# Performance work log

Measured on AMD Instinct MI355X. Metric: run time of the kernel, lower is better.

The kernel has to match this reference:

```python
import jax, jax.numpy as jnp
import numpy as np

D = 2048  # filter_dim
B = 4096  # tokens per TTT step


def setup_inputs() -> dict:
    key = jax.random.key(0)
    ks = jax.random.split(key, 8)
    s = 1.0 / np.sqrt(D)  # kaiming-ish scale so activations stay O(1)
    return {
        "src": jax.random.normal(ks[0], (B, D), jnp.float32),
        "theta_k": jax.random.normal(ks[1], (D, D), jnp.float32) * s,
        "theta_q": jax.random.normal(ks[2], (D, D), jnp.float32) * s,
        "theta_v": jax.random.normal(ks[3], (D, D), jnp.float32) * s,
        "W": jax.random.normal(ks[4], (D, D), jnp.float32) * s,
        "b": jnp.zeros((D,), jnp.float32),
        "lr_w": jax.random.uniform(ks[5], (D, D), jnp.float32) * 0.1,
        "lr_b": jax.random.uniform(ks[6], (D,), jnp.float32) * 0.1,
    }


def reference(src, theta_k, theta_q, theta_v, W, b, lr_w, lr_b):
    # Projections: src is [B, D], thetas are [D, D]
    train_view = src @ theta_k           # [B, D]
    label_view = src @ theta_v           # [B, D]
    test_view = src @ theta_q            # [B, D]

    target = label_view - train_view     # reconstruction target
    pred = train_view @ W.T + b          # nn.Linear(train_view)
    err = pred - target                  # [B, D]

    # Analytic grads of MSELoss (mean over B*D elements) wrt W ([D,D]) and b ([D])
    n = err.size  # B * D (static)
    coef = 2.0 / n
    gW = coef * (err.T @ train_view)     # [D, D], matches w.weight layout
    gb = coef * jnp.sum(err, axis=0)     # [D]

    # Per-element learning-rate SGD step (the in-place parameter rewrite)
    W_new = W - lr_w * gW
    b_new = b - lr_b * gb

    # Query with updated weights + residual
    z = test_view @ W_new.T + b_new + test_view
    return z
```

## Files before the change

### kernel.cpp

```cpp
#include <hip/hip_runtime.h>
#include <hip/hip_bf16.h>
#include <hip/hip_fp8.h>
#include <stdint.h>

#define D_DIM 2048
#define B_TOK 4096
#define COEF (2.0f / 8388608.0f)

typedef __bf16 bf16x8 __attribute__((ext_vector_type(8)));
typedef float  f32x4  __attribute__((ext_vector_type(4)));
typedef int    i32x8  __attribute__((ext_vector_type(8)));

__device__ __forceinline__ unsigned short f2bf(float f) {
  return __builtin_bit_cast(unsigned short, (__bf16)f);
}
__device__ __forceinline__ float bf2f(unsigned short u) {
  return (float)__builtin_bit_cast(__bf16, u);
}
__device__ __forceinline__ unsigned char f2f8(float f) {
  __hip_fp8_e4m3 v(f);
  return v.__x;
}

__device__ __forceinline__ void async16(const void* g, void* l) {
  __builtin_amdgcn_global_load_lds(
      (__attribute__((address_space(1))) void*)(g),
      (__attribute__((address_space(3))) void*)(l),
      16, 0, 0);
}

__device__ __forceinline__ void gemm_core_256(const unsigned short* __restrict__ Ablk,
                                              const unsigned short* __restrict__ Bblk,
                                              const int lda, const int ldb, const int KC,
                                              unsigned short* As, unsigned short* Bs,
                                              f32x4 acc[4][4]) {
  const int tid  = threadIdx.x;
  const int lane = tid & 63;
  const int wv   = tid >> 6;
  const int wm   = wv >> 1;
  const int wn   = wv & 1;
  const int t    = lane & 15;
  const int quad = lane >> 4;
  const int lrow = lane >> 3;
  const int kq   = lane & 7;
  const int kqs  = kq ^ lrow;

  const int nk = KC >> 6;

  auto stageA2 = [&](int buf, int kt, int l0) {
    const int k0 = kt << 6;
    unsigned short* Ad = As + buf * 16384;
#pragma unroll
    for (int l = l0; l < l0 + 2; ++l) {
      const int seg = wv * 4 + l;
      const int r   = seg * 8 + lrow;
      async16(Ablk + (size_t)r * lda + k0 + kqs * 8, Ad + seg * 512);
    }
  };
  auto stageB1 = [&](int buf, int kt, int l) {
    const int k0 = kt << 6;
    unsigned short* Bd = Bs + buf * 8192;
    const int seg = wv * 2 + l;
    const int r   = seg * 8 + lrow;
    async16(Bblk + (size_t)r * ldb + k0 + kqs * 8, Bd + seg * 512);
  };

  stageA2(0, 0, 0); stageA2(0, 0, 2); stageB1(0, 0, 0); stageB1(0, 0, 1);
  if (nk > 1) { stageA2(1, 1, 0); stageA2(1, 1, 2); stageB1(1, 1, 0); stageB1(1, 1, 1); }
  if (nk > 1) asm volatile("s_waitcnt vmcnt(6)" ::: "memory");
  else        asm volatile("s_waitcnt vmcnt(0)" ::: "memory");
  __builtin_amdgcn_s_barrier();

  int cur = 0;
  for (int kt = 0; kt < nk; ++kt) {
    const unsigned short* Ac = As + cur * 16384;
    const unsigned short* Bc = Bs + cur * 8192;
    const int nb = (cur >= 1) ? cur - 1 : 2;
    const bool pf = (kt + 2 < nk);

    bf16x8 af[4], bfr[4];
#pragma unroll
    for (int i = 0; i < 4; ++i) {
      const int rm = wm * 64 + i * 16 + t;
      af[i]  = *(const bf16x8*)(Ac + rm * 64 + ((quad) ^ (rm & 7)) * 8);
      const int rn = wn * 64 + i * 16 + t;
      bfr[i] = *(const bf16x8*)(Bc + rn * 64 + ((quad) ^ (rn & 7)) * 8);
    }
    __builtin_amdgcn_sched_barrier(0);
    if (pf) { stageA2(nb, kt + 2, 0); stageB1(nb, kt + 2, 0); }
    __builtin_amdgcn_sched_barrier(0);
    __builtin_amdgcn_s_barrier();
    asm volatile("s_waitcnt lgkmcnt(0)" ::: "memory");
    __builtin_amdgcn_sched_barrier(0);
    __builtin_amdgcn_s_setprio(1);
#pragma unroll
    for (int i = 0; i < 4; ++i)
#pragma unroll
      for (int j = 0; j < 4; ++j)
        acc[i][j] = __builtin_amdgcn_mfma_f32_16x16x32_bf16(af[i], bfr[j], acc[i][j], 0, 0, 0);
    __builtin_amdgcn_s_setprio(0);
    __builtin_amdgcn_sched_barrier(0);
    __builtin_amdgcn_s_barrier();

#pragma unroll
    for (int i = 0; i < 4; ++i) {
      const int rm = wm * 64 + i * 16 + t;
      af[i]  = *(const bf16x8*)(Ac + rm * 64 + ((4 + quad) ^ (rm & 7)) * 8);
      const int rn = wn * 64 + i * 16 + t;
      bfr[i] = *(const bf16x8*)(Bc + rn * 64 + ((4 + quad) ^ (rn & 7)) * 8);
    }
    __builtin_amdgcn_sched_barrier(0);
    if (pf) { stageA2(nb, kt + 2, 2); stageB1(nb, kt + 2, 1); }
    __builtin_amdgcn_sched_barrier(0);
    if (pf)               asm volatile("s_waitcnt vmcnt(6)" ::: "memory");
    else if (kt + 1 < nk) asm volatile("s_waitcnt vmcnt(0)" ::: "memory");
    __builtin_amdgcn_s_barrier();
    asm volatile("s_waitcnt lgkmcnt(0)" ::: "memory");
    __builtin_amdgcn_sched_barrier(0);
    __builtin_amdgcn_s_setprio(1);
#pragma unroll
    for (int i = 0; i < 4; ++i)
#pragma unroll
      for (int j = 0; j < 4; ++j)
        acc[i][j] = __builtin_amdgcn_mfma_f32_16x16x32_bf16(af[i], bfr[j], acc[i][j], 0, 0, 0);
    __builtin_amdgcn_s_setprio(0);
    __builtin_amdgcn_sched_barrier(0);
    __builtin_amdgcn_s_barrier();

    cur = (cur == 2) ? 0 : cur + 1;
  }
}

#define GEMM_PROLOGUE256(AP, BP, LDAv, LDBv, KCv)                              \
  __shared__ __align__(16) unsigned short As[3 * 16384];                       \
  __shared__ __align__(16) unsigned short Bs[3 * 8192];                        \
  const int lin = blockIdx.y * 16 + blockIdx.x;                                \
  const int swz = (lin & 7) * 32 + (lin >> 3);                                 \
  const int bx = swz & 15, by = swz >> 4;                                      \
  const unsigned short* Ablk = (AP) + (size_t)by * 256 * (LDAv);               \
  const unsigned short* Bblk = (BP) + (size_t)bx * 128 * (LDBv);               \
  f32x4 acc[4][4];                                                             \
  _Pragma("unroll") for (int i = 0; i < 4; ++i)                                \
  _Pragma("unroll") for (int j = 0; j < 4; ++j)                                \
      acc[i][j] = (f32x4){0.f, 0.f, 0.f, 0.f};                                 \
  gemm_core_256(Ablk, Bblk, (LDAv), (LDBv), (KCv), As, Bs, acc);               \
  const int lane = threadIdx.x & 63;                                           \
  const int wv = threadIdx.x >> 6;                                             \
  const int wm = wv >> 1, wn = wv & 1;                                         \
  const int t = lane & 15, quad = lane >> 4;                                   \
  const int gm_base = by * 256 + wm * 64;                                      \
  const int gn_base = bx * 128 + wn * 64;

__device__ __forceinline__ void gemm_core_f8_256(const unsigned char* __restrict__ Ablk,
                                                 const unsigned char* __restrict__ Bblk,
                                                 const int lda, const int ldb, const int KC,
                                                 unsigned char* As, unsigned char* Bs,
                                                 f32x4 acc[4][4]) {
  const int tid  = threadIdx.x;
  const int lane = tid & 63;
  const int wv   = tid >> 6;
  const int wm   = wv >> 1;
  const int wn   = wv & 1;
  const int t    = lane & 15;
  const int quad = lane >> 4;
  const int lrow = lane >> 3;
  const int kq   = lane & 7;
  const int kqs  = kq ^ lrow;

  const int nk = KC >> 7;

  auto stageA2 = [&](int buf, int kt, int l0) {
    const int k0 = kt << 7;
    unsigned char* Ad = As + buf * 32768;
#pragma unroll
    for (int l = l0; l < l0 + 2; ++l) {
      const int seg = wv * 4 + l;
      const int r   = seg * 8 + lrow;
      async16(Ablk + (size_t)r * lda + k0 + kqs * 16, Ad + seg * 1024);
    }
  };
  auto stageB1 = [&](int buf, int kt, int l) {
    const int k0 = kt << 7;
    unsigned char* Bd = Bs + buf * 16384;
    const int seg = wv * 2 + l;
    const int r   = seg * 8 + lrow;
    async16(Bblk + (size_t)r * ldb + k0 + kqs * 16, Bd + seg * 1024);
  };

  auto readF = [&](const unsigned char* base, int x) -> i32x8 {
    const uint4 lo = *(const uint4*)(base + (((quad << 1)    ) ^ x) * 16);
    const uint4 hi = *(const uint4*)(base + (((quad << 1) | 1) ^ x) * 16);
    return (i32x8){(int)lo.x, (int)lo.y, (int)lo.z, (int)lo.w,
                   (int)hi.x, (int)hi.y, (int)hi.z, (int)hi.w};
  };

  stageA2(0, 0, 0); stageA2(0, 0, 2); stageB1(0, 0, 0); stageB1(0, 0, 1);
  if (nk > 1) { stageA2(1, 1, 0); stageA2(1, 1, 2); stageB1(1, 1, 0); stageB1(1, 1, 1); }
  if (nk > 1) asm volatile("s_waitcnt vmcnt(6)" ::: "memory");
  else        asm volatile("s_waitcnt vmcnt(0)" ::: "memory");
  __builtin_amdgcn_s_barrier();

  int cur = 0;
  for (int kt = 0; kt < nk; ++kt) {
    const unsigned char* Ac = As + cur * 32768;
    const unsigned char* Bc = Bs + cur * 16384;
    const int nb = (cur >= 1) ? cur - 1 : 2;
    const bool pf = (kt + 2 < nk);

    i32x8 af[4], bq0, bq1;
#pragma unroll
    for (int i = 0; i < 4; ++i) {
      const int rm = wm * 64 + i * 16 + t;
      af[i] = readF(Ac + rm * 128, rm & 7);
    }
    {
      const int rn0 = wn * 64 + 0 * 16 + t;
      bq0 = readF(Bc + rn0 * 128, rn0 & 7);
      const int rn1 = wn * 64 + 1 * 16 + t;
      bq1 = readF(Bc + rn1 * 128, rn1 & 7);
    }
    __builtin_amdgcn_sched_barrier(0);
    if (pf) { stageA2(nb, kt + 2, 0); stageB1(nb, kt + 2, 0); }
    __builtin_amdgcn_sched_barrier(0);
    __builtin_amdgcn_s_barrier();
    asm volatile("s_waitcnt lgkmcnt(0)" ::: "memory");
    __builtin_amdgcn_sched_barrier(0);
    __builtin_amdgcn_s_setprio(1);
#pragma unroll
    for (int i = 0; i < 4; ++i) {
      acc[i][0] = __builtin_amdgcn_mfma_scale_f32_16x16x128_f8f6f4(
          af[i], bq0, acc[i][0], 0, 0, 0, 127, 0, 127);
      acc[i][1] = __builtin_amdgcn_mfma_scale_f32_16x16x128_f8f6f4(
          af[i], bq1, acc[i][1], 0, 0, 0, 127, 0, 127);
    }
    __builtin_amdgcn_s_setprio(0);
    __builtin_amdgcn_sched_barrier(0);
    __builtin_amdgcn_s_barrier();

    {
      const int rn2 = wn * 64 + 2 * 16 + t;
      bq0 = readF(Bc + rn2 * 128, rn2 & 7);
      const int rn3 = wn * 64 + 3 * 16 + t;
      bq1 = readF(Bc + rn3 * 128, rn3 & 7);
    }
    __builtin_amdgcn_sched_barrier(0);
    if (pf) { stageA2(nb, kt + 2, 2); stageB1(nb, kt + 2, 1); }
    __builtin_amdgcn_sched_barrier(0);
    if (pf)               asm volatile("s_waitcnt vmcnt(6)" ::: "memory");
    else if (kt + 1 < nk) asm volatile("s_waitcnt vmcnt(0)" ::: "memory");
    __builtin_amdgcn_s_barrier();
    asm volatile("s_waitcnt lgkmcnt(0)" ::: "memory");
    __builtin_amdgcn_sched_barrier(0);
    __builtin_amdgcn_s_setprio(1);
#pragma unroll
    for (int i = 0; i < 4; ++i) {
      acc[i][2] = __builtin_amdgcn_mfma_scale_f32_16x16x128_f8f6f4(
          af[i], bq0, acc[i][2], 0, 0, 0, 127, 0, 127);
      acc[i][3] = __builtin_amdgcn_mfma_scale_f32_16x16x128_f8f6f4(
          af[i], bq1, acc[i][3], 0, 0, 0, 127, 0, 127);
    }
    __builtin_amdgcn_s_setprio(0);
    __builtin_amdgcn_sched_barrier(0);
    __builtin_amdgcn_s_barrier();

    cur = (cur == 2) ? 0 : cur + 1;
  }
}

#define GEMM8_PROLOGUE256(AP, BP, LDAv, LDBv, KCv)                             \
  __shared__ __align__(16) unsigned char As8[3 * 32768];                       \
  __shared__ __align__(16) unsigned char Bs8[3 * 16384];                       \
  const int nwg = gridDim.x * gridDim.y;                                       \
  const int lin = blockIdx.y * 16 + blockIdx.x;                                \
  const int swz = (lin & 7) * (nwg >> 3) + (lin >> 3);                         \
  const int bx = swz & 15, by = swz >> 4;                                      \
  const unsigned char* Ablk = (AP) + (size_t)by * 256 * (LDAv);                \
  const unsigned char* Bblk = (BP) + (size_t)bx * 128 * (LDBv);                \
  f32x4 acc[4][4];                                                             \
  _Pragma("unroll") for (int i = 0; i < 4; ++i)                                \
  _Pragma("unroll") for (int j = 0; j < 4; ++j)                                \
      acc[i][j] = (f32x4){0.f, 0.f, 0.f, 0.f};                                 \
  gemm_core_f8_256(Ablk, Bblk, (LDAv), (LDBv), (KCv), As8, Bs8, acc);          \
  const int lane = threadIdx.x & 63;                                           \
  const int wv = threadIdx.x >> 6;                                             \
  const int wm = wv >> 1, wn = wv & 1;                                         \
  const int t = lane & 15, quad = lane >> 4;                                   \
  const int gm_base = by * 256 + wm * 64;                                      \
  const int gn_base = bx * 128 + wn * 64;

__global__ __launch_bounds__(512, 2) void gemm_train_f8(
    const unsigned char* __restrict__ srcA,
    const unsigned char* __restrict__ thkT8,
    unsigned char* __restrict__ src_cat_f8,
    unsigned char* __restrict__ trainT8) {
  GEMM8_PROLOGUE256(srcA, thkT8, 4096, 2048, 2048)
  unsigned char* scr = As8 + wv * 2304;
#pragma unroll
  for (int p = 0; p < 2; ++p) {
#pragma unroll
    for (int jl = 0; jl < 2; ++jl) {
      const int j = p * 2 + jl;
      const int gn = gn_base + j * 16 + t;
#pragma unroll
      for (int i = 0; i < 4; ++i) {
        const int gm0 = gm_base + i * 16 + quad * 4;
        uchar4 pk = make_uchar4(f2f8(acc[i][j][0]), f2f8(acc[i][j][1]),
                                f2f8(acc[i][j][2]), f2f8(acc[i][j][3]));
        src_cat_f8[(size_t)(gm0 + 0) * 4096 + gn] = pk.x;
        src_cat_f8[(size_t)(gm0 + 1) * 4096 + gn] = pk.y;
        src_cat_f8[(size_t)(gm0 + 2) * 4096 + gn] = pk.z;
        src_cat_f8[(size_t)(gm0 + 3) * 4096 + gn] = pk.w;
        *(uchar4*)(scr + (jl * 16 + t) * 72 + i * 16 + quad * 4) = pk;
      }
    }
    __syncthreads();
    const int row = lane >> 3, chunk = lane & 7;
#pragma unroll
    for (int q = 0; q < 4; ++q) {
      const int rr = q * 8 + row;
      const uint2 v = *(const uint2*)(scr + rr * 72 + chunk * 8);
      *(uint2*)(trainT8 + (size_t)(gn_base + p * 32 + rr) * B_TOK + gm_base + chunk * 8) = v;
    }
    __syncthreads();
  }
}

__global__ __launch_bounds__(512, 2) void gemm_test(
    const unsigned short* __restrict__ src_bf,
    const unsigned short* __restrict__ thqT,
    unsigned short* __restrict__ testv) {
  GEMM_PROLOGUE256(src_bf, thqT, 2048, 2048, 2048)
#pragma unroll
  for (int i = 0; i < 4; ++i) {
#pragma unroll
    for (int j = 0; j < 4; ++j) {
      const int gm0 = gm_base + i * 16 + quad * 4;
      const int gn  = gn_base + j * 16 + t;
#pragma unroll
      for (int r = 0; r < 4; ++r)
        testv[(size_t)(gm0 + r) * D_DIM + gn] = f2bf(acc[i][j][r]);
    }
  }
}

__global__ __launch_bounds__(512, 2) void gemm_err_f8(
    const unsigned char* __restrict__ src_cat_f8,
    const unsigned char* __restrict__ Wcat_f8,
    const float* __restrict__ bvec,
    unsigned char* __restrict__ errT8,
    float* __restrict__ gb) {
  GEMM8_PROLOGUE256(src_cat_f8, Wcat_f8, 4096, 4096, 4096)
  unsigned char* scr = As8 + wv * 2304;
#pragma unroll
  for (int p = 0; p < 2; ++p) {
#pragma unroll
    for (int jl = 0; jl < 2; ++jl) {
      const int j = p * 2 + jl;
      const int gn = gn_base + j * 16 + t;
      const float bias = bvec[gn];
      float cs = 0.f;
#pragma unroll
      for (int i = 0; i < 4; ++i) {
        const float e0 = acc[i][j][0] + bias, e1 = acc[i][j][1] + bias;
        const float e2 = acc[i][j][2] + bias, e3 = acc[i][j][3] + bias;
        *(uchar4*)(scr + (jl * 16 + t) * 72 + i * 16 + quad * 4) =
            make_uchar4(f2f8(e0), f2f8(e1), f2f8(e2), f2f8(e3));
        cs += e0 + e1 + e2 + e3;
      }
      cs += __shfl_xor(cs, 16);
      cs += __shfl_xor(cs, 32);
      if (quad == 0) atomicAdd(&gb[gn], cs);
    }
    __syncthreads();
    const int row = lane >> 3, chunk = lane & 7;
#pragma unroll
    for (int q = 0; q < 4; ++q) {
      const int rr = q * 8 + row;
      const uint2 v = *(const uint2*)(scr + rr * 72 + chunk * 8);
      *(uint2*)(errT8 + (size_t)(gn_base + p * 32 + rr) * B_TOK + gm_base + chunk * 8) = v;
    }
    __syncthreads();
  }
}

__global__ __launch_bounds__(512, 2) void gemm_gw_f8(
    const unsigned char* __restrict__ errT8,
    const unsigned char* __restrict__ trainT8,
    float* __restrict__ P0, float* __restrict__ P1) {
  const int z = blockIdx.z;
  const unsigned char* Abase = errT8 + z * 2048;
  const unsigned char* Bbase = trainT8 + z * 2048;
  GEMM8_PROLOGUE256(Abase, Bbase, B_TOK, B_TOK, 2048)
  float* P = (z == 0) ? P0 : P1;
#pragma unroll
  for (int i = 0; i < 4; ++i) {
#pragma unroll
    for (int j = 0; j < 4; ++j) {
      const int gm0 = gm_base + i * 16 + quad * 4;
      const int gn  = gn_base + j * 16 + t;
#pragma unroll
      for (int r = 0; r < 4; ++r)
        P[(size_t)(gm0 + r) * D_DIM + gn] = acc[i][j][r];
    }
  }
}

__global__ __launch_bounds__(256) void wnew_reduce(
    const float* __restrict__ P0, const float* __restrict__ P1,
    const float* __restrict__ W, const float* __restrict__ lr_w,
    unsigned short* __restrict__ Wnew) {
  const int i = blockIdx.x * 256 + threadIdx.x;
  const float4 p0 = ((const float4*)P0)[i];
  const float4 p1 = ((const float4*)P1)[i];
  const float4 w  = ((const float4*)W)[i];
  const float4 l  = ((const float4*)lr_w)[i];
  ((ushort4*)Wnew)[i] = make_ushort4(
      f2bf(w.x - l.x * (COEF * (p0.x + p1.x))),
      f2bf(w.y - l.y * (COEF * (p0.y + p1.y))),
      f2bf(w.z - l.z * (COEF * (p0.z + p1.z))),
      f2bf(w.w - l.w * (COEF * (p0.w + p1.w))));
}

__global__ __launch_bounds__(512, 2) void gemm_out(
    const unsigned short* __restrict__ testv,
    const unsigned short* __restrict__ Wnew,
    const float* __restrict__ bvec,
    const float* __restrict__ lr_b,
    const float* __restrict__ gb,
    float* __restrict__ out) {
  GEMM_PROLOGUE256(testv, Wnew, 2048, 2048, 2048)
#pragma unroll
  for (int j = 0; j < 4; ++j) {
    const int gn = gn_base + j * 16 + t;
    const float bias = bvec[gn] - lr_b[gn] * (COEF * gb[gn]);
#pragma unroll
    for (int i = 0; i < 4; ++i) {
      const int gm0 = gm_base + i * 16 + quad * 4;
#pragma unroll
      for (int r = 0; r < 4; ++r) {
        const size_t idx = (size_t)(gm0 + r) * D_DIM + gn;
        out[idx] = acc[i][j][r] + bias + bf2f(testv[idx]);
      }
    }
  }
}

__global__ __launch_bounds__(256) void cvt_all(const float* __restrict__ src,
                                               const float* __restrict__ W,
                                               unsigned short* __restrict__ src_bf,
                                               unsigned char* __restrict__ src_cat_f8,
                                               unsigned char* __restrict__ Wcat_f8,
                                               float* __restrict__ gb) {
  const int i = blockIdx.x * 256 + threadIdx.x;
  if (i < 512) ((float4*)gb)[i] = (float4){0.f, 0.f, 0.f, 0.f};
  if (i < 2097152) {
    const int m = i >> 9, c = i & 511;
    const float4 v = ((const float4*)src)[i];
    ((ushort4*)src_bf)[i] = make_ushort4(f2bf(v.x), f2bf(v.y), f2bf(v.z), f2bf(v.w));
    *(uchar4*)(src_cat_f8 + (size_t)m * 4096 + 2048 + c * 4) =
        make_uchar4(f2f8(v.x), f2f8(v.y), f2f8(v.z), f2f8(v.w));
  } else {
    const int j = i - 2097152;
    const int n = j >> 9, c = j & 511;
    const float4 v = ((const float4*)W)[j];
    *(uchar4*)(Wcat_f8 + (size_t)n * 4096 + c * 4) =
        make_uchar4(f2f8(v.x), f2f8(v.y), f2f8(v.z), f2f8(v.w));
  }
}

__global__ __launch_bounds__(256) void tcvt(
    const float* __restrict__ thk, const float* __restrict__ thq,
    const float* __restrict__ thv,
    unsigned char* __restrict__ thkT8, unsigned short* __restrict__ thqT,
    unsigned char* __restrict__ Wcat_f8) {
  __shared__ float tile[32][33];
  const int z = blockIdx.z;
  const int bx = blockIdx.x * 32, by = blockIdx.y * 32;
  const int tx = threadIdx.x & 31, ty = threadIdx.x >> 5;
#pragma unroll
  for (int l = 0; l < 4; ++l) {
    const int r = ty + l * 8;
    const size_t idx = (size_t)(by + r) * D_DIM + bx + tx;
    tile[r][tx] = (z == 0) ? thk[idx] : (z == 1) ? thq[idx] : (thk[idx] - thv[idx]);
  }
  __syncthreads();
#pragma unroll
  for (int l = 0; l < 4; ++l) {
    const int r = ty + l * 8;
    if (z == 0)
      thkT8[(size_t)(bx + r) * 2048 + by + tx] = f2f8(tile[tx][r]);
    else if (z == 1)
      thqT[(size_t)(bx + r) * 2048 + by + tx] = f2bf(tile[tx][r]);
    else
      Wcat_f8[(size_t)(bx + r) * 4096 + 2048 + by + tx] = f2f8(tile[tx][r]);
  }
}

extern "C" void kernel_launch(void* const* d_in, const int* in_sizes, int n_in,
                              void* d_out, int out_size, void* d_ws, size_t ws_size,
                              hipStream_t stream) {
  const float* src = (const float*)d_in[0];
  const float* thk = (const float*)d_in[1];
  const float* thq = (const float*)d_in[2];
  const float* thv = (const float*)d_in[3];
  const float* W   = (const float*)d_in[4];
  const float* bv  = (const float*)d_in[5];
  const float* lrw = (const float*)d_in[6];
  const float* lrb = (const float*)d_in[7];
  float* out = (float*)d_out;

  char* ws = (char*)d_ws;
  const size_t MB = 1024 * 1024;
  unsigned short* src_bf     = (unsigned short*)(ws + 0);
  unsigned char*  src_cat_f8 = (unsigned char*)(ws + 16 * MB);
  unsigned char*  Wcat_f8    = (unsigned char*)(ws + 32 * MB);
  unsigned char*  thkT8      = (unsigned char*)(ws + 40 * MB);
  unsigned short* thqT       = (unsigned short*)(ws + 44 * MB);
  unsigned char*  trainT8    = (unsigned char*)(ws + 52 * MB);
  unsigned short* testv      = (unsigned short*)(ws + 60 * MB);
  unsigned char*  errT8      = (unsigned char*)(ws + 76 * MB);
  unsigned short* WnewBf     = (unsigned short*)(ws + 84 * MB);
  float*          P0         = (float*)(ws + 92 * MB);
  float*          P1         = (float*)(ws + 108 * MB);
  float*          gb         = (float*)(ws + 124 * MB);

  cvt_all<<<12288, 256, 0, stream>>>(src, W, src_bf, src_cat_f8, Wcat_f8, gb);
  tcvt<<<dim3(64, 64, 3), 256, 0, stream>>>(thk, thq, thv, thkT8, thqT, Wcat_f8);

  gemm_train_f8<<<dim3(16, 16), 512, 0, stream>>>(src_cat_f8 + 2048, thkT8,
                                                  src_cat_f8, trainT8);
  gemm_test<<<dim3(16, 16), 512, 0, stream>>>(src_bf, thqT, testv);
  gemm_err_f8<<<dim3(16, 16), 512, 0, stream>>>(src_cat_f8, Wcat_f8, bv, errT8, gb);
  gemm_gw_f8<<<dim3(16, 8, 2), 512, 0, stream>>>(errT8, trainT8, P0, P1);
  wnew_reduce<<<4096, 256, 0, stream>>>(P0, P1, W, lrw, WnewBf);
  gemm_out<<<dim3(16, 16), 512, 0, stream>>>(testv, WnewBf, bv, lrb, gb, out);
}
```

Measured before the change: 335.7 us.

## Cut barriers per k-step by reading full LDS tile before MFMA phases

In both the bf16 and fp8 GEMM cores, each k-iteration now reads all fragments for both sub-phases from LDS up front, issues all global prefetches at once, and runs the two MFMA groups separated only by partial lgkmcnt waits. This takes the per-iteration workgroup barriers from four down to one. It is meant to remove barrier stalls and let LDS reads overlap the first MFMA group. The cost is higher register pressure from the doubled fragment arrays. Safety with the triple buffer now depends on the single remaining barrier.

```diff
diff --git a/kernel.cpp b/kernel.cpp
--- a/kernel.cpp
+++ b/kernel.cpp
@@ -78,55 +78,49 @@
     const int nb = (cur >= 1) ? cur - 1 : 2;
     const bool pf = (kt + 2 < nk);
 
-    bf16x8 af[4], bfr[4];
+    bf16x8 af0[4], bf0[4], af1[4], bf1[4];
 #pragma unroll
     for (int i = 0; i < 4; ++i) {
       const int rm = wm * 64 + i * 16 + t;
-      af[i]  = *(const bf16x8*)(Ac + rm * 64 + ((quad) ^ (rm & 7)) * 8);
       const int rn = wn * 64 + i * 16 + t;
-      bfr[i] = *(const bf16x8*)(Bc + rn * 64 + ((quad) ^ (rn & 7)) * 8);
-    }
-    __builtin_amdgcn_sched_barrier(0);
-    if (pf) { stageA2(nb, kt + 2, 0); stageB1(nb, kt + 2, 0); }
-    __builtin_amdgcn_sched_barrier(0);
-    __builtin_amdgcn_s_barrier();
-    asm volatile("s_waitcnt lgkmcnt(0)" ::: "memory");
-    __builtin_amdgcn_sched_barrier(0);
-    __builtin_amdgcn_s_setprio(1);
-#pragma unroll
-    for (int i = 0; i < 4; ++i)
-#pragma unroll
-      for (int j = 0; j < 4; ++j)
-        acc[i][j] = __builtin_amdgcn_mfma_f32_16x16x32_bf16(af[i], bfr[j], acc[i][j], 0, 0, 0);
-    __builtin_amdgcn_s_setprio(0);
-    __builtin_amdgcn_sched_barrier(0);
-    __builtin_amdgcn_s_barrier();
-
+      af0[i] = *(const bf16x8*)(Ac + rm * 64 + ((quad) ^ (rm & 7)) * 8);
+      bf0[i] = *(const bf16x8*)(Bc + rn * 64 + ((quad) ^ (rn & 7)) * 8);
+    }
+    __builtin_amdgcn_sched_barrier(0);
 #pragma unroll
     for (int i = 0; i < 4; ++i) {
       const int rm = wm * 64 + i * 16 + t;
-      af[i]  = *(const bf16x8*)(Ac + rm * 64 + ((4 + quad) ^ (rm & 7)) * 8);
       const int rn = wn * 64 + i * 16 + t;
-      bfr[i] = *(const bf16x8*)(Bc + rn * 64 + ((4 + quad) ^ (rn & 7)) * 8);
-    }
-    __builtin_amdgcn_sched_barrier(0);
-    if (pf) { stageA2(nb, kt + 2, 2); stageB1(nb, kt + 2, 1); }
+      af1[i] = *(const bf16x8*)(Ac + rm * 64 + ((4 + quad) ^ (rm & 7)) * 8);
+      bf1[i] = *(const bf16x8*)(Bc + rn * 64 + ((4 + quad) ^ (rn & 7)) * 8);
+    }
+    __builtin_amdgcn_sched_barrier(0);
+    if (pf) { stageA2(nb, kt + 2, 0); stageA2(nb, kt + 2, 2);
+              stageB1(nb, kt + 2, 0); stageB1(nb, kt + 2, 1); }
+    __builtin_amdgcn_sched_barrier(0);
+    asm volatile("s_waitcnt lgkmcnt(8)" ::: "memory");
+    __builtin_amdgcn_sched_barrier(0);
+    __builtin_amdgcn_s_setprio(1);
+#pragma unroll
+    for (int i = 0; i < 4; ++i)
+#pragma unroll
+      for (int j = 0; j < 4; ++j)
+        acc[i][j] = __builtin_amdgcn_mfma_f32_16x16x32_bf16(af0[i], bf0[j], acc[i][j], 0, 0, 0);
+    __builtin_amdgcn_s_setprio(0);
+    __builtin_amdgcn_sched_barrier(0);
+    asm volatile("s_waitcnt lgkmcnt(0)" ::: "memory");
+    __builtin_amdgcn_sched_barrier(0);
+    __builtin_amdgcn_s_setprio(1);
+#pragma unroll
+    for (int i = 0; i < 4; ++i)
+#pragma unroll
+      for (int j = 0; j < 4; ++j)
+        acc[i][j] = __builtin_amdgcn_mfma_f32_16x16x32_bf16(af1[i], bf1[j], acc[i][j], 0, 0, 0);
+    __builtin_amdgcn_s_setprio(0);
     __builtin_amdgcn_sched_barrier(0);
     if (pf)               asm volatile("s_waitcnt vmcnt(6)" ::: "memory");
     else if (kt + 1 < nk) asm volatile("s_waitcnt vmcnt(0)" ::: "memory");
     __builtin_amdgcn_s_barrier();
-    asm volatile("s_waitcnt lgkmcnt(0)" ::: "memory");
-    __builtin_amdgcn_sched_barrier(0);
-    __builtin_amdgcn_s_setprio(1);
-#pragma unroll
-    for (int i = 0; i < 4; ++i)
-#pragma unroll
-      for (int j = 0; j < 4; ++j)
-        acc[i][j] = __builtin_amdgcn_mfma_f32_16x16x32_bf16(af[i], bfr[j], acc[i][j], 0, 0, 0);
-    __builtin_amdgcn_s_setprio(0);
-    __builtin_amdgcn_sched_barrier(0);
-    __builtin_amdgcn_s_barrier();
-
     cur = (cur == 2) ? 0 : cur + 1;
   }
 }
@@ -207,7 +201,7 @@
     const int nb = (cur >= 1) ? cur - 1 : 2;
     const bool pf = (kt + 2 < nk);
 
-    i32x8 af[4], bq0, bq1;
+    i32x8 af[4], bq0, bq1, bq2, bq3;
 #pragma unroll
     for (int i = 0; i < 4; ++i) {
       const int rm = wm * 64 + i * 16 + t;
@@ -220,10 +214,17 @@
       bq1 = readF(Bc + rn1 * 128, rn1 & 7);
     }
     __builtin_amdgcn_sched_barrier(0);
-    if (pf) { stageA2(nb, kt + 2, 0); stageB1(nb, kt + 2, 0); }
-    __builtin_amdgcn_sched_barrier(0);
-    __builtin_amdgcn_s_barrier();
-    asm volatile("s_waitcnt lgkmcnt(0)" ::: "memory");
+    {
+      const int rn2 = wn * 64 + 2 * 16 + t;
+      bq2 = readF(Bc + rn2 * 128, rn2 & 7);
+      const int rn3 = wn * 64 + 3 * 16 + t;
+      bq3 = readF(Bc + rn3 * 128, rn3 & 7);
+    }
+    __builtin_amdgcn_sched_barrier(0);
+    if (pf) { stageA2(nb, kt + 2, 0); stageA2(nb, kt + 2, 2);
+              stageB1(nb, kt + 2, 0); stageB1(nb, kt + 2, 1); }
+    __builtin_amdgcn_sched_barrier(0);
+    asm volatile("s_waitcnt lgkmcnt(4)" ::: "memory");
     __builtin_amdgcn_sched_barrier(0);
     __builtin_amdgcn_s_setprio(1);
 #pragma unroll
@@ -235,34 +236,21 @@
     }
     __builtin_amdgcn_s_setprio(0);
     __builtin_amdgcn_sched_barrier(0);
-    __builtin_amdgcn_s_barrier();
-
-    {
-      const int rn2 = wn * 64 + 2 * 16 + t;
-      bq0 = readF(Bc + rn2 * 128, rn2 & 7);
-      const int rn3 = wn * 64 + 3 * 16 + t;
-      bq1 = readF(Bc + rn3 * 128, rn3 & 7);
-    }
-    __builtin_amdgcn_sched_barrier(0);
-    if (pf) { stageA2(nb, kt + 2, 2); stageB1(nb, kt + 2, 1); }
+    asm volatile("s_waitcnt lgkmcnt(0)" ::: "memory");
+    __builtin_amdgcn_sched_barrier(0);
+    __builtin_amdgcn_s_setprio(1);
+#pragma unroll
+    for (int i = 0; i < 4; ++i) {
+      acc[i][2] = __builtin_amdgcn_mfma_scale_f32_16x16x128_f8f6f4(
+          af[i], bq2, acc[i][2], 0, 0, 0, 127, 0, 127);
+      acc[i][3] = __builtin_amdgcn_mfma_scale_f32_16x16x128_f8f6f4(
+          af[i], bq3, acc[i][3], 0, 0, 0, 127, 0, 127);
+    }
+    __builtin_amdgcn_s_setprio(0);
     __builtin_amdgcn_sched_barrier(0);
     if (pf)               asm volatile("s_waitcnt vmcnt(6)" ::: "memory");
     else if (kt + 1 < nk) asm volatile("s_waitcnt vmcnt(0)" ::: "memory");
     __builtin_amdgcn_s_barrier();
-    asm volatile("s_waitcnt lgkmcnt(0)" ::: "memory");
-    __builtin_amdgcn_sched_barrier(0);
-    __builtin_amdgcn_s_setprio(1);
-#pragma unroll
-    for (int i = 0; i < 4; ++i) {
-      acc[i][2] = __builtin_amdgcn_mfma_scale_f32_16x16x128_f8f6f4(
-          af[i], bq0, acc[i][2], 0, 0, 0, 127, 0, 127);
-      acc[i][3] = __builtin_amdgcn_mfma_scale_f32_16x16x128_f8f6f4(
-          af[i], bq1, acc[i][3], 0, 0, 0, 127, 0, 127);
-    }
-    __builtin_amdgcn_s_setprio(0);
-    __builtin_amdgcn_sched_barrier(0);
-    __builtin_amdgcn_s_barrier();
-
     cur = (cur == 2) ? 0 : cur + 1;
   }
 }
```

After: 323.3 us. 3.7% less time.
